# Optimization experiments

Measured on AMD Instinct MI355X. Metric: run time of the kernel, lower is better.

Reference implementation:

```python
import jax, jax.numpy as jnp
import numpy as np

RAD2DEG = 180.0 / 3.14159  # module uses 3.14159, not pi

def _conv2d(x, w):
    # x: (N,1,H,W), w: (O,1,3,3), SAME padding, stride 1
    return jax.lax.conv_general_dilated(
        x, w, window_strides=(1, 1), padding='SAME',
        dimension_numbers=('NCHW', 'OIHW', 'NCHW'))

def _make_filters():
    sobel = np.array([[1, 0, -1], [2, 0, -2], [1, 0, -1]], dtype=np.float32)
    f0   = [[0,0,0],[0,1,-1],[0,0,0]]
    f45  = [[0,0,0],[0,1,0],[0,0,-1]]
    f90  = [[0,0,0],[0,1,0],[0,-1,0]]
    f135 = [[0,0,0],[0,1,0],[-1,0,0]]
    f180 = [[0,0,0],[-1,1,0],[0,0,0]]
    f225 = [[-1,0,0],[0,1,0],[0,0,0]]
    f270 = [[0,-1,0],[0,1,0],[0,0,0]]
    f315 = [[0,0,-1],[0,1,0],[0,0,0]]
    dirs = np.stack([f0,f45,f90,f135,f180,f225,f270,f315]).astype(np.float32)
    return sobel, dirs

def setup_inputs() -> dict:
    key = jax.random.key(0)
    H, W = 2160, 3840
    img = jax.random.uniform(key, (1, 3, H, W), dtype=jnp.float32)
    sobel, dirs = _make_filters()
    sobel_h = jnp.asarray(sobel)[None, None]          # (1,1,3,3)
    sobel_v = jnp.asarray(sobel.T)[None, None]        # (1,1,3,3)
    dir_w = jnp.asarray(dirs)[:, None]                # (8,1,3,3)
    return {"img": img, "sobel_h": sobel_h, "sobel_v": sobel_v, "dir_w": dir_w}

def reference(img, sobel_h, sobel_v, dir_w):
    # grayscale: mean of the 3 channels
    gray = (img[:, 0:1] + img[:, 1:2] + img[:, 2:3]) / 3.0        # (1,1,H,W)
    grad_x = _conv2d(gray, sobel_h)
    grad_y = _conv2d(gray, sobel_v)
    grad_mag = jnp.sqrt(grad_x ** 2 + grad_y ** 2)                # (1,1,H,W)
    # orientation in degrees, snapped to multiples of 45 (round-half-even, like torch.round)
    ori = jnp.round((jnp.arctan2(grad_y, grad_x) * RAD2DEG + 180.0) / 45.0)
    idx_pos = jnp.mod(ori, 8.0).astype(jnp.int32)                 # (1,1,H,W)
    idx_neg = jnp.mod(ori + 4.0, 8.0).astype(jnp.int32)
    all_filtered = _conv2d(grad_mag, dir_w)                       # (1,8,H,W)
    # per-pixel channel select (the flattened gather in the original)
    pos = jnp.take_along_axis(all_filtered, idx_pos, axis=1)      # (1,1,H,W)
    neg = jnp.take_along_axis(all_filtered, idx_neg, axis=1)
    is_max = jnp.minimum(pos, neg) > 0.0
    # in-place aliasing in the original: thin_edges/early_threshold alias grad_mag,
    # so the final binary map is: is_max AND (grad_mag >= 0.2)
    th = jnp.where(is_max & (grad_mag >= 0.2), 1.0, 0.0).astype(jnp.float32)
    return th
```

## Files before the change

kernel.cpp:

```cpp
#include <hip/hip_runtime.h>
#include <math.h>

#define IMG_W 3840
#define IMG_H 2160
#define OUTW  60
#define R     20
#define ITERS (R + 4)
#define MROWS (R + 2)

#define DXPACK 0x901A
#define DYPACK 0x1A9

#define T1_SLOPE 0.41421317376456f
#define T2_SLOPE 2.41420676743300f
#define SECT_EPS 3.0e-5f

__device__ __noinline__ int slow_sector(float sx, float sy) {
#pragma clang fp contract(off)
    const float RADF = (float)(180.0 / 3.14159);
    float t = atan2f(sy, sx);
    float wv = ((t * RADF) + 180.0f) / 45.0f;
    float ori = rintf(wv);
    float fr = fabsf(wv - ori);
    if (fr > 0.4995f) {
        double td = atan2((double)sy, (double)sx);
        float t2 = (float)td;
        wv = ((t2 * RADF) + 180.0f) / 45.0f;
        ori = rintf(wv);
    }
    return ((int)ori) & 7;
}

__global__ __launch_bounds__(256, 4) void canny_like_kernel(const float* __restrict__ img,
                                                            float* __restrict__ out) {
#pragma clang fp contract(off)
    __shared__ float lds_m[4][MROWS][64];

    const int lane = threadIdx.x;
    const int w    = threadIdx.y;
    const int X0   = (blockIdx.x * 4 + w) * OUTW;
    const int Y0   = blockIdx.y * R;
    const int x    = X0 - 2 + lane;
    const bool xok    = (unsigned)x < (unsigned)IMG_W;
    const int  xc     = min(max(x, 0), IMG_W - 1);
    const bool xmok   = (lane >= 1) && (lane <= 62) && xok;
    const bool xoutok = (lane >= 2) && (lane <= 61);

    const float* im1 = img + (size_t)IMG_W * IMG_H;
    const float* im2 = img + 2 * (size_t)IMG_W * IMG_H;

    float gl[3], gc[3], gr[3];
    float mc_p = 0.0f;
    int   off_p = 0;

#pragma unroll
    for (int k = 0; k < ITERS; ++k) {
        const int y = Y0 - 2 + k;
        float g = 0.0f;
        if ((unsigned)y < (unsigned)IMG_H) {
            int o = y * IMG_W + xc;
            float c0 = img[o], c1 = im1[o], c2 = im2[o];
            float t = ((c0 + c1) + c2) / 3.0f;
            g = xok ? t : 0.0f;
        }
        const int s = k % 3;
        gc[s] = g;
        gl[s] = __shfl_up(g, 1);
        gr[s] = __shfl_down(g, 1);

        if (k >= 2) {
            const int i0 = (k - 2) % 3, i1 = (k - 1) % 3, i2 = k % 3;
            float a00 = gl[i0], a01 = gc[i0], a02 = gr[i0];
            float a10 = gl[i1],               a12 = gr[i1];
            float a20 = gl[i2], a21 = gc[i2], a22 = gr[i2];
            float sx = a00;
            sx = sx - a02;
            sx = sx + 2.0f * a10;
            sx = sx - 2.0f * a12;
            sx = sx + a20;
            sx = sx - a22;
            float sy = a00;
            sy = sy + 2.0f * a01;
            sy = sy + a02;
            sy = sy - a20;
            sy = sy - 2.0f * a21;
            sy = sy - a22;
            float magv = sqrtf(sx * sx + sy * sy);

            float ax = fabsf(sx), ay = fabsf(sy);
            float d1 = fmaf(-T1_SLOPE, ax, ay);
            float d2 = fmaf(-T2_SLOPE, ax, ay);
            float sA = ax + ay;
            int dxo, dyo;
            if (__builtin_expect(fabsf(d1) < SECT_EPS * sA || fabsf(d2) < SECT_EPS * sA, 0)) {
                int idx = slow_sector(sx, sy);
                dxo = ((DXPACK >> (2 * idx)) & 3) - 1;
                dyo = ((DYPACK >> (2 * idx)) & 3) - 1;
            } else {
                dxo = (d2 > 0.0f) ? 0 : ((sx > 0.0f) ? -1 : 1);
                dyo = (d1 < 0.0f) ? 0 : ((sy > 0.0f) ? -1 : 1);
            }
            const bool vok = xmok && ((unsigned)(y - 1) < (unsigned)IMG_H);
            float mag = vok ? magv : 0.0f;
            int  offv = vok ? (dyo * 64 + dxo) : 0;

            lds_m[w][k - 2][lane] = mag;

            if (k >= 4) {
                const float* cb = &lds_m[w][k - 3][lane];
                float mp = cb[off_p];
                float mn = cb[-off_p];
                float res = (fminf(mc_p - mp, mc_p - mn) > 0.0f && mc_p >= 0.2f) ? 1.0f : 0.0f;
                if (xoutok)
                    out[(size_t)(Y0 + k - 4) * IMG_W + x] = res;
            }
            mc_p = mag;
            off_p = offv;
        }
    }
}

extern "C" void kernel_launch(void* const* d_in, const int* in_sizes, int n_in,
                              void* d_out, int out_size, void* d_ws, size_t ws_size,
                              hipStream_t stream) {
    const float* img = (const float*)d_in[0];
    float* out = (float*)d_out;
    dim3 grid(64 / 4, IMG_H / R);
    dim3 block(64, 4);
    canny_like_kernel<<<grid, block, 0, stream>>>(img, out);
}
```

Before: 166.3 us.

## Process two pixels per lane and defer ambiguous-sector pixels to a fixup kernel

New measurement: 188.6 us. +13.4%, slower.

```diff
diff --git a/kernel.cpp b/kernel.cpp
--- a/kernel.cpp
+++ b/kernel.cpp
@@ -3,17 +3,16 @@
 
 #define IMG_W 3840
 #define IMG_H 2160
-#define OUTW  60
+#define OUTW  120
 #define R     20
 #define ITERS (R + 4)
-#define MROWS (R + 2)
 
 #define DXPACK 0x901A
 #define DYPACK 0x1A9
-
 #define T1_SLOPE 0.41421317376456f
 #define T2_SLOPE 2.41420676743300f
 #define SECT_EPS 3.0e-5f
+#define FIX_CAP  (1u << 22)
 
 __device__ __noinline__ int slow_sector(float sx, float sy) {
 #pragma clang fp contract(off)
@@ -31,92 +30,207 @@
     return ((int)ori) & 7;
 }
 
-__global__ __launch_bounds__(256, 4) void canny_like_kernel(const float* __restrict__ img,
-                                                            float* __restrict__ out) {
-#pragma clang fp contract(off)
-    __shared__ float lds_m[4][MROWS][64];
+__global__ void zero_counter(unsigned* fix) { if (threadIdx.x == 0) fix[0] = 0u; }
+
+__global__ __launch_bounds__(256, 3) void canny_main(const float* __restrict__ img,
+                                                     float* __restrict__ out,
+                                                     unsigned* __restrict__ fix) {
+#pragma clang fp contract(off)
+    __shared__ float ring[4 * 512];
 
     const int lane = threadIdx.x;
-    const int w    = threadIdx.y;
-    const int X0   = (blockIdx.x * 4 + w) * OUTW;
-    const int Y0   = blockIdx.y * R;
-    const int x    = X0 - 2 + lane;
-    const bool xok    = (unsigned)x < (unsigned)IMG_W;
-    const int  xc     = min(max(x, 0), IMG_W - 1);
-    const bool xmok   = (lane >= 1) && (lane <= 62) && xok;
-    const bool xoutok = (lane >= 2) && (lane <= 61);
-
-    const float* im1 = img + (size_t)IMG_W * IMG_H;
-    const float* im2 = img + 2 * (size_t)IMG_W * IMG_H;
-
-    float gl[3], gc[3], gr[3];
-    float mc_p = 0.0f;
-    int   off_p = 0;
+    const int wv   = threadIdx.y;
+    float* rbase = ring + wv * 512;
+
+    const int strip = blockIdx.x * 4 + wv;
+    const int X0 = strip * OUTW;
+    const int Y0 = blockIdx.y * R;
+    const int r0 = 2 * lane;
+    const int x0 = X0 - 2 + r0;
+    const int x1 = x0 + 1;
+    const bool xk0 = (unsigned)x0 < (unsigned)IMG_W;
+    const bool xk1 = (unsigned)x1 < (unsigned)IMG_W;
+    const bool outok = (lane >= 1) && (lane <= 60);
+    const int  rb = outok ? r0 : 2;
+    const int  xc = min(max(x0, 0), IMG_W - 2);
+
+    const float* p0 = img + xc;
+    const float* p1 = p0 + (size_t)IMG_W * IMG_H;
+    const float* p2 = p1 + (size_t)IMG_W * IMG_H;
+
+    float GL[3], G0[3], G1[3], GR[3];
+    float mc0 = 0.f, mc1 = 0.f;
+    int dx0 = 0, dy0 = 0, dx1 = 0, dy1 = 0;
 
 #pragma unroll
     for (int k = 0; k < ITERS; ++k) {
         const int y = Y0 - 2 + k;
-        float g = 0.0f;
-        if ((unsigned)y < (unsigned)IMG_H) {
-            int o = y * IMG_W + xc;
-            float c0 = img[o], c1 = im1[o], c2 = im2[o];
-            float t = ((c0 + c1) + c2) / 3.0f;
-            g = xok ? t : 0.0f;
-        }
+        const bool yok = (unsigned)y < (unsigned)IMG_H;
+        const int yc = min(max(y, 0), IMG_H - 1);
+        const size_t o = (size_t)yc * IMG_W;
+        const float2 A = *(const float2*)(p0 + o);
+        const float2 B = *(const float2*)(p1 + o);
+        const float2 C = *(const float2*)(p2 + o);
+        float t0 = ((A.x + B.x) + C.x) / 3.0f;
+        float t1 = ((A.y + B.y) + C.y) / 3.0f;
         const int s = k % 3;
-        gc[s] = g;
-        gl[s] = __shfl_up(g, 1);
-        gr[s] = __shfl_down(g, 1);
+        float g0 = (yok && xk0) ? t0 : 0.0f;
+        float g1 = (yok && xk1) ? t1 : 0.0f;
+        G0[s] = g0;
+        G1[s] = g1;
+        GL[s] = __shfl_up(g1, 1);
+        GR[s] = __shfl_down(g0, 1);
 
         if (k >= 2) {
             const int i0 = (k - 2) % 3, i1 = (k - 1) % 3, i2 = k % 3;
-            float a00 = gl[i0], a01 = gc[i0], a02 = gr[i0];
-            float a10 = gl[i1],               a12 = gr[i1];
-            float a20 = gl[i2], a21 = gc[i2], a22 = gr[i2];
-            float sx = a00;
-            sx = sx - a02;
-            sx = sx + 2.0f * a10;
-            sx = sx - 2.0f * a12;
-            sx = sx + a20;
-            sx = sx - a22;
-            float sy = a00;
-            sy = sy + 2.0f * a01;
-            sy = sy + a02;
-            sy = sy - a20;
-            sy = sy - 2.0f * a21;
-            sy = sy - a22;
-            float magv = sqrtf(sx * sx + sy * sy);
-
-            float ax = fabsf(sx), ay = fabsf(sy);
-            float d1 = fmaf(-T1_SLOPE, ax, ay);
-            float d2 = fmaf(-T2_SLOPE, ax, ay);
-            float sA = ax + ay;
-            int dxo, dyo;
-            if (__builtin_expect(fabsf(d1) < SECT_EPS * sA || fabsf(d2) < SECT_EPS * sA, 0)) {
-                int idx = slow_sector(sx, sy);
-                dxo = ((DXPACK >> (2 * idx)) & 3) - 1;
-                dyo = ((DYPACK >> (2 * idx)) & 3) - 1;
-            } else {
-                dxo = (d2 > 0.0f) ? 0 : ((sx > 0.0f) ? -1 : 1);
-                dyo = (d1 < 0.0f) ? 0 : ((sy > 0.0f) ? -1 : 1);
+            const int m = y - 1;
+            const bool mok = (unsigned)m < (unsigned)IMG_H;
+
+            float sx0 = GL[i0];
+            sx0 = sx0 - G1[i0];
+            sx0 = sx0 + 2.0f * GL[i1];
+            sx0 = sx0 - 2.0f * G1[i1];
+            sx0 = sx0 + GL[i2];
+            sx0 = sx0 - G1[i2];
+            float sy0 = GL[i0];
+            sy0 = sy0 + 2.0f * G0[i0];
+            sy0 = sy0 + G1[i0];
+            sy0 = sy0 - GL[i2];
+            sy0 = sy0 - 2.0f * G0[i2];
+            sy0 = sy0 - G1[i2];
+            float mag0 = sqrtf(sx0 * sx0 + sy0 * sy0);
+
+            float sx1 = G0[i0];
+            sx1 = sx1 - GR[i0];
+            sx1 = sx1 + 2.0f * G0[i1];
+            sx1 = sx1 - 2.0f * GR[i1];
+            sx1 = sx1 + G0[i2];
+            sx1 = sx1 - GR[i2];
+            float sy1 = G0[i0];
+            sy1 = sy1 + 2.0f * G1[i0];
+            sy1 = sy1 + GR[i0];
+            sy1 = sy1 - G0[i2];
+            sy1 = sy1 - 2.0f * G1[i2];
+            sy1 = sy1 - GR[i2];
+            float mag1 = sqrtf(sx1 * sx1 + sy1 * sy1);
+
+            float M0 = (mok && xk0) ? mag0 : 0.0f;
+            float M1 = (mok && xk1) ? mag1 : 0.0f;
+
+            float ax0 = fabsf(sx0), ay0 = fabsf(sy0);
+            float d10 = fmaf(-T1_SLOPE, ax0, ay0);
+            float d20 = fmaf(-T2_SLOPE, ax0, ay0);
+            float sA0 = ax0 + ay0;
+            int ndx0 = (d20 > 0.0f) ? 0 : ((sx0 > 0.0f) ? -1 : 1);
+            int ndy0 = (d10 < 0.0f) ? 0 : ((sy0 > 0.0f) ? -1 : 1);
+            bool inb0 = (fabsf(d10) < SECT_EPS * sA0) || (fabsf(d20) < SECT_EPS * sA0);
+
+            float ax1 = fabsf(sx1), ay1 = fabsf(sy1);
+            float d11 = fmaf(-T1_SLOPE, ax1, ay1);
+            float d21 = fmaf(-T2_SLOPE, ax1, ay1);
+            float sA1 = ax1 + ay1;
+            int ndx1 = (d21 > 0.0f) ? 0 : ((sx1 > 0.0f) ? -1 : 1);
+            int ndy1 = (d11 < 0.0f) ? 0 : ((sy1 > 0.0f) ? -1 : 1);
+            bool inb1 = (fabsf(d11) < SECT_EPS * sA1) || (fabsf(d21) < SECT_EPS * sA1);
+
+            bool f0 = inb0 && outok && (M0 >= 0.2f);
+            bool f1 = inb1 && outok && (M1 >= 0.2f);
+            if (f0 || f1) {
+                if (f0) {
+                    unsigned id = atomicAdd(fix, 1u);
+                    if (id < FIX_CAP) fix[1 + id] = ((unsigned)m << 12) | (unsigned)x0;
+                }
+                if (f1) {
+                    unsigned id = atomicAdd(fix, 1u);
+                    if (id < FIX_CAP) fix[1 + id] = ((unsigned)m << 12) | (unsigned)x1;
+                }
             }
-            const bool vok = xmok && ((unsigned)(y - 1) < (unsigned)IMG_H);
-            float mag = vok ? magv : 0.0f;
-            int  offv = vok ? (dyo * 64 + dxo) : 0;
-
-            lds_m[w][k - 2][lane] = mag;
+
+            float* wr = rbase + ((k - 2) & 3) * 128;
+            *(float2*)(wr + r0) = make_float2(M0, M1);
 
             if (k >= 4) {
-                const float* cb = &lds_m[w][k - 3][lane];
-                float mp = cb[off_p];
-                float mn = cb[-off_p];
-                float res = (fminf(mc_p - mp, mc_p - mn) > 0.0f && mc_p >= 0.2f) ? 1.0f : 0.0f;
-                if (xoutok)
-                    out[(size_t)(Y0 + k - 4) * IMG_W + x] = res;
+                const int n = m - 1;
+                float* bA = rbase + ((k - 4) & 3) * 128;
+                float* bB = rbase + ((k - 3) & 3) * 128;
+                float* bC = rbase + ((k - 2) & 3) * 128;
+                float* bp0 = (dy0 < 0) ? bA : ((dy0 > 0) ? bC : bB);
+                float* bn0 = (dy0 < 0) ? bC : ((dy0 > 0) ? bA : bB);
+                float* bp1 = (dy1 < 0) ? bA : ((dy1 > 0) ? bC : bB);
+                float* bn1 = (dy1 < 0) ? bC : ((dy1 > 0) ? bA : bB);
+                float mp0 = bp0[rb + dx0];
+                float mn0 = bn0[rb - dx0];
+                float mp1 = bp1[rb + 1 + dx1];
+                float mn1 = bn1[rb + 1 - dx1];
+                float r0v = (fminf(mc0 - mp0, mc0 - mn0) > 0.0f && mc0 >= 0.2f) ? 1.0f : 0.0f;
+                float r1v = (fminf(mc1 - mp1, mc1 - mn1) > 0.0f && mc1 >= 0.2f) ? 1.0f : 0.0f;
+                if (outok)
+                    *(float2*)(out + (size_t)n * IMG_W + x0) = make_float2(r0v, r1v);
             }
-            mc_p = mag;
-            off_p = offv;
+            mc0 = M0; mc1 = M1;
+            dx0 = ndx0; dy0 = ndy0; dx1 = ndx1; dy1 = ndy1;
         }
+    }
+}
+
+__device__ __forceinline__ float gray_at(const float* img, int xx, int yy) {
+#pragma clang fp contract(off)
+    if ((unsigned)xx >= (unsigned)IMG_W || (unsigned)yy >= (unsigned)IMG_H) return 0.0f;
+    size_t o = (size_t)yy * IMG_W + xx;
+    float c0 = img[o];
+    float c1 = img[o + (size_t)IMG_W * IMG_H];
+    float c2 = img[o + 2 * (size_t)IMG_W * IMG_H];
+    return ((c0 + c1) + c2) / 3.0f;
+}
+
+__device__ void sobel_at(const float* img, int xx, int yy, float& sxo, float& syo) {
+#pragma clang fp contract(off)
+    float a00 = gray_at(img, xx - 1, yy - 1), a01 = gray_at(img, xx, yy - 1), a02 = gray_at(img, xx + 1, yy - 1);
+    float a10 = gray_at(img, xx - 1, yy),                                     a12 = gray_at(img, xx + 1, yy);
+    float a20 = gray_at(img, xx - 1, yy + 1), a21 = gray_at(img, xx, yy + 1), a22 = gray_at(img, xx + 1, yy + 1);
+    float s = a00;
+    s = s - a02;
+    s = s + 2.0f * a10;
+    s = s - 2.0f * a12;
+    s = s + a20;
+    s = s - a22;
+    sxo = s;
+    float t = a00;
+    t = t + 2.0f * a01;
+    t = t + a02;
+    t = t - a20;
+    t = t - 2.0f * a21;
+    t = t - a22;
+    syo = t;
+}
+
+__device__ float mag_at(const float* img, int xx, int yy) {
+#pragma clang fp contract(off)
+    if ((unsigned)xx >= (unsigned)IMG_W || (unsigned)yy >= (unsigned)IMG_H) return 0.0f;
+    float sx, sy;
+    sobel_at(img, xx, yy, sx, sy);
+    return sqrtf(sx * sx + sy * sy);
+}
+
+__global__ void canny_fixup(const float* __restrict__ img, float* __restrict__ out,
+                            const unsigned* __restrict__ fix) {
+#pragma clang fp contract(off)
+    unsigned cnt = fix[0];
+    if (cnt > FIX_CAP) cnt = FIX_CAP;
+    for (unsigned i = blockIdx.x * blockDim.x + threadIdx.x; i < cnt;
+         i += gridDim.x * blockDim.x) {
+        unsigned pk = fix[1 + i];
+        int xx = (int)(pk & 4095u), yy = (int)(pk >> 12);
+        float sx, sy;
+        sobel_at(img, xx, yy, sx, sy);
+        int idx = slow_sector(sx, sy);
+        int dxo = ((DXPACK >> (2 * idx)) & 3) - 1;
+        int dyo = ((DYPACK >> (2 * idx)) & 3) - 1;
+        float mc = sqrtf(sx * sx + sy * sy);
+        float mp = mag_at(img, xx + dxo, yy + dyo);
+        float mn = mag_at(img, xx - dxo, yy - dyo);
+        out[(size_t)yy * IMG_W + xx] =
+            (fminf(mc - mp, mc - mn) > 0.0f && mc >= 0.2f) ? 1.0f : 0.0f;
     }
 }
 
@@ -125,7 +239,8 @@
                               hipStream_t stream) {
     const float* img = (const float*)d_in[0];
     float* out = (float*)d_out;
-    dim3 grid(64 / 4, IMG_H / R);
-    dim3 block(64, 4);
-    canny_like_kernel<<<grid, block, 0, stream>>>(img, out);
-}
+    unsigned* fix = (unsigned*)d_ws;
+    zero_counter<<<1, 64, 0, stream>>>(fix);
+    canny_main<<<dim3(8, IMG_H / R), dim3(64, 4), 0, stream>>>(img, out, fix);
+    canny_fixup<<<dim3(16), dim3(256), 0, stream>>>(img, out, fix);
+}
```
